# Kernel optimization log

Hardware: AMD Instinct MI355X
Metric: run time of the kernel (lower is better)

Reference implementation:

```python
import jax, jax.numpy as jnp
import numpy as np

NUM_GENES = 20000
NUM_CLASS = 32
BATCH_SIZE = 8
N = NUM_GENES * BATCH_SIZE      # 160_000 total nodes
E = 2_560_000                    # edges (avg degree 16)
K = 10
ALPHA = 0.1


def setup_inputs() -> dict:
    key = jax.random.key(0)
    ks = jax.random.split(key, 9)
    x = jax.random.normal(ks[0], (N, 1), dtype=jnp.float32)
    edge_index = jax.random.randint(ks[1], (2, E), 0, N, dtype=jnp.int32)
    batch = jnp.repeat(jnp.arange(BATCH_SIZE, dtype=jnp.int32), NUM_GENES)
    exp_emb_table = jax.random.normal(ks[2], (NUM_GENES, NUM_CLASS), dtype=jnp.float32) * 0.1
    exp_bias_table = jax.random.normal(ks[3], (NUM_GENES, 1), dtype=jnp.float32) * 0.1
    s = 1.0 / np.sqrt(NUM_CLASS)
    W1 = jax.random.uniform(ks[4], (NUM_CLASS, NUM_CLASS), jnp.float32, -s, s)
    b1 = jax.random.uniform(ks[5], (NUM_CLASS,), jnp.float32, -s, s)
    W2 = jax.random.uniform(ks[6], (NUM_CLASS, NUM_CLASS), jnp.float32, -s, s)
    b2 = jax.random.uniform(ks[7], (NUM_CLASS,), jnp.float32, -s, s)
    return {"x": x, "edge_index": edge_index, "batch": batch,
            "exp_emb_table": exp_emb_table, "exp_bias_table": exp_bias_table,
            "W1": W1, "b1": b1, "W2": W2, "b2": b2}


def reference(x, edge_index, batch, exp_emb_table, exp_bias_table, W1, b1, W2, b2):
    # node_index tiles 0..num_genes-1 for each graph in the batch
    node_index = jnp.tile(jnp.arange(NUM_GENES), BATCH_SIZE)        # [N]
    h = exp_emb_table[node_index] * x + exp_bias_table[node_index]  # [N, C]
    # dropout is identity in eval mode
    h = jax.nn.relu(h @ W1.T + b1)
    h = h @ W2.T + b2

    # APPNP: gcn_norm with self-loops, then k power-iteration steps
    loops = jnp.arange(N, dtype=edge_index.dtype)
    row = jnp.concatenate([edge_index[0], loops])  # source
    col = jnp.concatenate([edge_index[1], loops])  # target
    deg = jax.ops.segment_sum(jnp.ones_like(col, dtype=h.dtype), col, num_segments=N)
    dinv = jnp.where(deg > 0, jax.lax.rsqrt(deg), 0.0)
    norm = (dinv[row] * dinv[col])[:, None]        # [E+N, 1]

    h0 = h
    def step(carry, _):
        agg = jax.ops.segment_sum(carry[row] * norm, col, num_segments=N)
        return (1.0 - ALPHA) * agg + ALPHA * h0, None
    h, _ = jax.lax.scan(step, h, None, length=K)

    # global mean pool over graphs
    sums = jax.ops.segment_sum(h, batch, num_segments=BATCH_SIZE)
    counts = jax.ops.segment_sum(jnp.ones((N, 1), h.dtype), batch, num_segments=BATCH_SIZE)
    return sums / counts  # [BATCH_SIZE, NUM_CLASS]
```

## Files before the change

### kernel.cpp

```cpp
#include <hip/hip_runtime.h>

typedef unsigned int u32;
typedef unsigned short u16;

#define NPB 64
#define CNTB 512
#define MSEG 16
#define PCHUNK 4096
#define SPB 16
#define DHCHUNK 8
#define OUT_CHUNK 640

__device__ inline float bf2f(u16 b) { return __uint_as_float(((u32)b) << 16); }
__device__ inline u16 f2bf(float f) {
    u32 u = __float_as_uint(f);
    return (u16)((u + 0x7fffu + ((u >> 16) & 1u)) >> 16);
}
__device__ inline u32 pack2(float a, float b) { return (u32)f2bf(a) | ((u32)f2bf(b) << 16); }

__global__ void k_zero_i(int* __restrict__ p, int n) {
    int i = blockIdx.x * 256 + threadIdx.x;
    if (i < n) p[i] = 0;
}

__global__ void k_cnt(const int* __restrict__ ei, int E,
                      int* __restrict__ pcnt, int nbuckets) {
    extern __shared__ int h[];
    int M = nbuckets + 64;
    for (int i = threadIdx.x; i < M; i += 256) h[i] = 0;
    __syncthreads();
    int stride = gridDim.x * 256;
    for (int e = blockIdx.x * 256 + threadIdx.x; e < E; e += stride) {
        atomicAdd(&h[ei[e] >> 6], 1);
        atomicAdd(&h[nbuckets + (ei[E + e] >> 12)], 1);
    }
    __syncthreads();
    int* dst = pcnt + (size_t)blockIdx.x * M;
    for (int i = threadIdx.x; i < M; i += 256) dst[i] = h[i];
}

__global__ void k_merge(const int* __restrict__ pcnt, int M, int nbuckets,
                        int* __restrict__ bcnt, int* __restrict__ dscnt) {
    int bin = blockIdx.x * 256 + threadIdx.x;
    if (bin >= M) return;
    const int per = CNTB / MSEG;
    const int* p = pcnt + (size_t)(blockIdx.y * per) * M + bin;
    int s0 = 0, s1 = 0, s2 = 0, s3 = 0;
    #pragma unroll
    for (int b = 0; b < per; b += 4) {
        s0 += p[(size_t)(b + 0) * M];
        s1 += p[(size_t)(b + 1) * M];
        s2 += p[(size_t)(b + 2) * M];
        s3 += p[(size_t)(b + 3) * M];
    }
    int s = s0 + s1 + s2 + s3;
    if (s) {
        if (bin < nbuckets) atomicAdd(&bcnt[bin], s);
        else atomicAdd(&dscnt[bin - nbuckets], s);
    }
}

__global__ void k_scanB(const int* __restrict__ bcnt, int nbuckets,
                        const int* __restrict__ dscnt,
                        int* __restrict__ boff, int* __restrict__ bCur,
                        int* __restrict__ soff, int* __restrict__ sCur,
                        int* __restrict__ dsoff, int* __restrict__ dsCur,
                        int* __restrict__ offsets, int N, int E, int nsup, int nsupD) {
    __shared__ int s[1024];
    __shared__ int carry;
    int t = threadIdx.x;
    if (t == 0) carry = 0;
    __syncthreads();
    for (int base = 0; base < nbuckets; base += 1024) {
        int i = base + t;
        int v = (i < nbuckets) ? bcnt[i] : 0;
        s[t] = v;
        __syncthreads();
        for (int off = 1; off < 1024; off <<= 1) {
            int tmp = (t >= off) ? s[t - off] : 0;
            __syncthreads();
            s[t] += tmp;
            __syncthreads();
        }
        int pos = s[t] - v + carry;
        if (i < nbuckets) {
            boff[i] = pos;
            bCur[i] = pos;
            if ((i & 63) == 0) { soff[i >> 6] = pos; sCur[i >> 6] = pos; }
        }
        __syncthreads();
        if (t == 1023) carry += s[1023];
        __syncthreads();
    }
    if (t == 0) {
        boff[nbuckets] = E; soff[nsup] = E; offsets[N] = E;
        int acc = 0;
        for (int i = 0; i < nsupD; ++i) {
            dsoff[i] = acc; dsCur[i] = acc;
            acc += dscnt[i];
        }
        dsoff[nsupD] = E;
    }
}

__global__ __launch_bounds__(512) void k_part(const int* __restrict__ ei, int E,
                                              int* __restrict__ sCur, int* __restrict__ dsCur,
                                              u32* __restrict__ buf1, u16* __restrict__ dbuf) {
    __shared__ int cnt[64];
    __shared__ int cur[64];
    __shared__ int dcnt[64];
    __shared__ int dcur[64];
    int c0 = blockIdx.x * PCHUNK;
    int c1 = min(E, c0 + PCHUNK);
    int t = threadIdx.x;
    if (t < 64) { cnt[t] = 0; dcnt[t] = 0; }
    __syncthreads();
    for (int e = c0 + t; e < c1; e += 512) {
        atomicAdd(&cnt[ei[e] >> 12], 1);
        atomicAdd(&dcnt[ei[E + e] >> 12], 1);
    }
    __syncthreads();
    if (t < 64) {
        int c = cnt[t];
        cur[t] = c ? atomicAdd(&sCur[t], c) : 0;
        int dc = dcnt[t];
        dcur[t] = dc ? atomicAdd(&dsCur[t], dc) : 0;
    }
    __syncthreads();
    for (int e = c0 + t; e < c1; e += 512) {
        int s = ei[e];
        int d = ei[E + e];
        int p = atomicAdd(&cur[s >> 12], 1);
        buf1[p] = (u32)(d & 0x3FFFF) | ((u32)(s & 4095) << 18);
        int pd = atomicAdd(&dcur[d >> 12], 1);
        dbuf[pd] = (u16)(d & 4095);
    }
}

__global__ __launch_bounds__(256) void k_dhist(const u16* __restrict__ dbuf,
                                               const int* __restrict__ dsoff,
                                               int* __restrict__ deg, int N) {
    __shared__ int h[4096];
    int sup = blockIdx.x / DHCHUNK;
    int ch = blockIdx.x % DHCHUNK;
    int t = threadIdx.x;
    for (int i = t; i < 4096; i += 256) h[i] = 0;
    __syncthreads();
    int s0 = dsoff[sup], s1 = dsoff[sup + 1];
    int per = (s1 - s0 + DHCHUNK - 1) / DHCHUNK;
    int c0 = s0 + ch * per;
    int c1 = min(s1, c0 + per);
    for (int e = c0 + t; e < c1; e += 256)
        atomicAdd(&h[dbuf[e]], 1);
    __syncthreads();
    int vbase = sup << 12;
    for (int i = t; i < 4096; i += 256) {
        int v = h[i];
        if (v && vbase + i < N) atomicAdd(&deg[vbase + i], v);
    }
}

__global__ __launch_bounds__(256) void k_p2(const u32* __restrict__ buf1,
                                            const int* __restrict__ soff,
                                            int* __restrict__ bCur,
                                            u32* __restrict__ binned) {
    __shared__ int cnt[64];
    __shared__ int cur[64];
    int sb = blockIdx.x / SPB;
    int ch = blockIdx.x % SPB;
    int s0 = soff[sb], s1 = soff[sb + 1];
    int per = (s1 - s0 + SPB - 1) / SPB;
    int c0 = s0 + ch * per;
    int c1 = min(s1, c0 + per);
    int t = threadIdx.x;
    if (t < 64) cnt[t] = 0;
    __syncthreads();
    for (int e = c0 + t; e < c1; e += 256)
        atomicAdd(&cnt[(buf1[e] >> 24) & 63], 1);
    __syncthreads();
    if (t < 64) {
        int c = cnt[t];
        cur[t] = (c > 0) ? atomicAdd(&bCur[(sb << 6) + t], c) : 0;
    }
    __syncthreads();
    for (int e = c0 + t; e < c1; e += 256) {
        u32 v = buf1[e];
        int p = atomicAdd(&cur[(v >> 24) & 63], 1);
        binned[p] = v & 0x00FFFFFFu;
    }
}

__global__ __launch_bounds__(256) void k_sort(const u32* __restrict__ binned,
                                              const int* __restrict__ boff,
                                              int* __restrict__ offsets,
                                              int* __restrict__ dsts, int N) {
    __shared__ int cnt[64];
    __shared__ int off[64];
    int b = blockIdx.x;
    int s0 = boff[b], s1 = boff[b + 1];
    int t = threadIdx.x;
    if (t < 64) cnt[t] = 0;
    __syncthreads();
    for (int e = s0 + t; e < s1; e += 256)
        atomicAdd(&cnt[(binned[e] >> 18) & 63], 1);
    __syncthreads();
    if (t == 0) {
        int acc = s0;
        #pragma unroll
        for (int i = 0; i < 64; ++i) { off[i] = acc; acc += cnt[i]; }
    }
    __syncthreads();
    int vbase = b << 6;
    if (t < 64 && vbase + t < N) offsets[vbase + t] = off[t];
    __syncthreads();
    if (t < 64) cnt[t] = off[t];
    __syncthreads();
    for (int e = s0 + t; e < s1; e += 256) {
        u32 v = binned[e];
        int p = atomicAdd(&cnt[(v >> 18) & 63], 1);
        dsts[p] = (int)(v & 0x3FFFFu);
    }
}

__global__ __launch_bounds__(256) void k_AW(const float* __restrict__ emb,
                                            const float* __restrict__ W1,
                                            float* __restrict__ A,
                                            float* __restrict__ s1, int ngenes) {
    __shared__ float w1[32][33];
    __shared__ float eb[8][33];
    int t = threadIdx.x;
    int j = t & 31, gl = t >> 5;
    for (int i = t; i < 1024; i += 256) w1[i >> 5][i & 31] = W1[i];
    int g = blockIdx.x * 8 + gl;
    if (g < ngenes) eb[gl][j] = emb[g * 32 + j];
    __syncthreads();
    if (blockIdx.x == 0 && t < 32) {
        float acc = 0.f;
        #pragma unroll
        for (int c = 0; c < 32; ++c) acc += w1[t][c];
        s1[t] = acc;
    }
    if (g < ngenes) {
        float acc = 0.f;
        #pragma unroll
        for (int c = 0; c < 32; ++c) acc = fmaf(eb[gl][c], w1[j][c], acc);
        A[(size_t)g * 32 + j] = acc;
    }
}

__global__ __launch_bounds__(256) void k_h0(const float* __restrict__ x,
                                            const float* __restrict__ A,
                                            const float* __restrict__ bias,
                                            const float* __restrict__ s1,
                                            const float* __restrict__ b1,
                                            const float* __restrict__ W2,
                                            const float* __restrict__ b2,
                                            const int* __restrict__ deg,
                                            float* __restrict__ dinv,
                                            float* __restrict__ afac,
                                            float* __restrict__ rd,
                                            uint4* __restrict__ h0,
                                            uint4* __restrict__ q0,
                                            float* __restrict__ out, int out_n,
                                            int N, int ngenes) {
    int node = blockIdx.x * 256 + threadIdx.x;
    if (blockIdx.x == 0 && threadIdx.x < out_n) out[threadIdx.x] = 0.f;
    if (node >= N) return;
    float d = (float)(deg[node] + 1);
    float dv = rsqrtf(d);
    dinv[node] = dv;
    afac[node] = 0.9f * dv * dv;
    rd[node] = sqrtf(d);
    int g = node % ngenes;
    float xv = x[node];
    float bv = bias[g];
    const float4* Ar = (const float4*)(A + (size_t)g * 32);
    float r1[32];
    #pragma unroll
    for (int q = 0; q < 8; ++q) {
        float4 a4 = Ar[q];
        r1[q * 4 + 0] = fmaxf(fmaf(xv, a4.x, fmaf(bv, s1[q * 4 + 0], b1[q * 4 + 0])), 0.f);
        r1[q * 4 + 1] = fmaxf(fmaf(xv, a4.y, fmaf(bv, s1[q * 4 + 1], b1[q * 4 + 1])), 0.f);
        r1[q * 4 + 2] = fmaxf(fmaf(xv, a4.z, fmaf(bv, s1[q * 4 + 2], b1[q * 4 + 2])), 0.f);
        r1[q * 4 + 3] = fmaxf(fmaf(xv, a4.w, fmaf(bv, s1[q * 4 + 3], b1[q * 4 + 3])), 0.f);
    }
    u32 ow[16];
    #pragma unroll
    for (int i = 0; i < 32; i += 2) {
        float accA = b2[i];
        float accB = b2[i + 1];
        #pragma unroll
        for (int j2 = 0; j2 < 32; ++j2) {
            accA = fmaf(r1[j2], W2[i * 32 + j2], accA);
            accB = fmaf(r1[j2], W2[(i + 1) * 32 + j2], accB);
        }
        ow[i >> 1] = pack2(accA, accB);
    }
    #pragma unroll
    for (int q = 0; q < 4; ++q) {
        uint4 o;
        o.x = ow[q * 4 + 0];
        o.y = ow[q * 4 + 1];
        o.z = ow[q * 4 + 2];
        o.w = ow[q * 4 + 3];
        h0[(size_t)node * 4 + q] = o;
    }
    int gb = node / ngenes;
    u32 lo = (u32)f2bf(dv);
    u32 hi = lo << 16;
    uint4 qo;
    qo.x = (gb == 0) ? lo : (gb == 1) ? hi : 0u;
    qo.y = (gb == 2) ? lo : (gb == 3) ? hi : 0u;
    qo.z = (gb == 4) ? lo : (gb == 5) ? hi : 0u;
    qo.w = (gb == 6) ? lo : (gb == 7) ? hi : 0u;
    q0[node] = qo;
}

__device__ inline void qacc(const uint4& v, float& c0, float& c1, float& c2, float& c3,
                            float& c4, float& c5, float& c6, float& c7) {
    c0 += bf2f((u16)v.x); c1 += bf2f((u16)(v.x >> 16));
    c2 += bf2f((u16)v.y); c3 += bf2f((u16)(v.y >> 16));
    c4 += bf2f((u16)v.z); c5 += bf2f((u16)(v.z >> 16));
    c6 += bf2f((u16)v.w); c7 += bf2f((u16)(v.w >> 16));
}

__global__ __launch_bounds__(256) void k_prop8(const uint4* __restrict__ qin,
                                               uint4* __restrict__ qout,
                                               const float* __restrict__ a,
                                               const float* __restrict__ dinv,
                                               const int* __restrict__ offsets,
                                               const int* __restrict__ dsts,
                                               int N, int ngenes) {
    int node = blockIdx.x * 256 + threadIdx.x;
    if (node >= N) return;
    int s0 = offsets[node];
    int s1 = offsets[node + 1];
    uint4 self = qin[node];
    float c0 = bf2f((u16)self.x), c1 = bf2f((u16)(self.x >> 16));
    float c2 = bf2f((u16)self.y), c3 = bf2f((u16)(self.y >> 16));
    float c4 = bf2f((u16)self.z), c5 = bf2f((u16)(self.z >> 16));
    float c6 = bf2f((u16)self.w), c7 = bf2f((u16)(self.w >> 16));
    int e = s0;
    for (; e + 8 <= s1; e += 8) {
        int d0 = dsts[e + 0], d1 = dsts[e + 1], d2 = dsts[e + 2], d3 = dsts[e + 3];
        int d4 = dsts[e + 4], d5 = dsts[e + 5], d6 = dsts[e + 6], d7 = dsts[e + 7];
        uint4 v0 = qin[d0];
        uint4 v1 = qin[d1];
        uint4 v2 = qin[d2];
        uint4 v3 = qin[d3];
        uint4 v4 = qin[d4];
        uint4 v5 = qin[d5];
        uint4 v6 = qin[d6];
        uint4 v7 = qin[d7];
        qacc(v0, c0, c1, c2, c3, c4, c5, c6, c7);
        qacc(v1, c0, c1, c2, c3, c4, c5, c6, c7);
        qacc(v2, c0, c1, c2, c3, c4, c5, c6, c7);
        qacc(v3, c0, c1, c2, c3, c4, c5, c6, c7);
        qacc(v4, c0, c1, c2, c3, c4, c5, c6, c7);
        qacc(v5, c0, c1, c2, c3, c4, c5, c6, c7);
        qacc(v6, c0, c1, c2, c3, c4, c5, c6, c7);
        qacc(v7, c0, c1, c2, c3, c4, c5, c6, c7);
    }
    if (e + 4 <= s1) {
        int d0 = dsts[e + 0], d1 = dsts[e + 1], d2 = dsts[e + 2], d3 = dsts[e + 3];
        uint4 v0 = qin[d0];
        uint4 v1 = qin[d1];
        uint4 v2 = qin[d2];
        uint4 v3 = qin[d3];
        qacc(v0, c0, c1, c2, c3, c4, c5, c6, c7);
        qacc(v1, c0, c1, c2, c3, c4, c5, c6, c7);
        qacc(v2, c0, c1, c2, c3, c4, c5, c6, c7);
        qacc(v3, c0, c1, c2, c3, c4, c5, c6, c7);
        e += 4;
    }
    for (; e < s1; ++e) {
        uint4 v = qin[dsts[e]];
        qacc(v, c0, c1, c2, c3, c4, c5, c6, c7);
    }
    float av = a[node];
    float qi = 0.1f * dinv[node];
    int gb = node / ngenes;
    c0 = av * c0 + ((gb == 0) ? qi : 0.f);
    c1 = av * c1 + ((gb == 1) ? qi : 0.f);
    c2 = av * c2 + ((gb == 2) ? qi : 0.f);
    c3 = av * c3 + ((gb == 3) ? qi : 0.f);
    c4 = av * c4 + ((gb == 4) ? qi : 0.f);
    c5 = av * c5 + ((gb == 5) ? qi : 0.f);
    c6 = av * c6 + ((gb == 6) ? qi : 0.f);
    c7 = av * c7 + ((gb == 7) ? qi : 0.f);
    uint4 o;
    o.x = pack2(c0, c1);
    o.y = pack2(c2, c3);
    o.z = pack2(c4, c5);
    o.w = pack2(c6, c7);
    qout[node] = o;
}

__global__ __launch_bounds__(256) void k_out(const uint4* __restrict__ q,
                                             const u16* __restrict__ h0,
                                             const float* __restrict__ rd,
                                             float* __restrict__ out,
                                             int N, int ngenes) {
    __shared__ float wq[64][8];
    __shared__ u16 hs[64][32];
    int t = threadIdx.x;
    int b = t >> 5, c = t & 31;
    float acc = 0.f;
    int base = blockIdx.x * OUT_CHUNK;
    int lim = min(N, base + OUT_CHUNK);
    for (int v0 = base; v0 < lim; v0 += 64) {
        int nv = min(64, lim - v0);
        __syncthreads();
        int r = t >> 2, w4 = t & 3;
        if (r < nv) {
            *(uint4*)&hs[r][w4 * 8] = ((const uint4*)(h0 + (size_t)(v0 + r) * 32))[w4];
            u32 wv = ((const u32*)&q[v0 + r])[w4];
            float rdv = rd[v0 + r];
            wq[r][w4 * 2] = bf2f((u16)wv) * rdv;
            wq[r][w4 * 2 + 1] = bf2f((u16)(wv >> 16)) * rdv;
        }
        __syncthreads();
        for (int i = 0; i < nv; ++i)
            acc = fmaf(wq[i][b], bf2f(hs[i][c]), acc);
    }
    atomicAdd(&out[b * 32 + c], acc / (float)ngenes);
}

extern "C" void kernel_launch(void* const* d_in, const int* in_sizes, int n_in,
                              void* d_out, int out_size, void* d_ws, size_t ws_size,
                              hipStream_t stream) {
    const float* x    = (const float*)d_in[0];
    const int*   ei   = (const int*)d_in[1];
    const float* emb  = (const float*)d_in[3];
    const float* bias = (const float*)d_in[4];
    const float* W1   = (const float*)d_in[5];
    const float* b1   = (const float*)d_in[6];
    const float* W2   = (const float*)d_in[7];
    const float* b2   = (const float*)d_in[8];
    float* out = (float*)d_out;

    int N = in_sizes[0];
    int E = in_sizes[1] / 2;
    int ngenes = in_sizes[4];
    int nbuckets = (N + NPB - 1) / NPB;
    int nsup = (nbuckets + 63) / 64;
    int nsupD = (N + 4095) / 4096;
    int M = nbuckets + 64;

    char* pws = (char*)d_ws;
    auto carve = [&](size_t bytes) {
        void* r = (void*)pws;
        pws += (bytes + 255) & ~(size_t)255;
        return r;
    };
    u16*   h0      = (u16*)carve((size_t)N * 32 * 2);
    uint4* qA      = (uint4*)carve((size_t)N * 16);
    uint4* qB      = (uint4*)carve((size_t)N * 16);
    float* Amat    = (float*)carve((size_t)ngenes * 32 * 4);
    float* s1v     = (float*)carve(32 * 4);
    float* dinv    = (float*)carve((size_t)N * 4);
    float* afac    = (float*)carve((size_t)N * 4);
    float* rd      = (float*)carve((size_t)N * 4);
    int*   offsets = (int*)carve((size_t)(N + 1) * 4);
    int*   deg     = (int*)carve((size_t)N * 4);
    int*   bcnt    = (int*)carve((size_t)nbuckets * 4);
    int*   dscnt   = (int*)carve(64 * 4);
    int*   boff    = (int*)carve((size_t)(nbuckets + 1) * 4);
    int*   bCur    = (int*)carve((size_t)nbuckets * 4);
    int*   soff    = (int*)carve(65 * 4);
    int*   sCur    = (int*)carve(64 * 4);
    int*   dsoff   = (int*)carve(65 * 4);
    int*   dsCur   = (int*)carve(64 * 4);
    int*   pcnt    = (int*)carve((size_t)CNTB * M * 4);
    u32*   buf1    = (u32*)carve((size_t)E * 4);
    u32*   binned  = (u32*)carve((size_t)E * 4);
    int*   dsts    = (int*)carve((size_t)E * 4);
    u16*   dbuf    = (u16*)carve((size_t)E * 2);

    int nbN = (N + 255) / 256;
    int zlen = (int)(dscnt - deg) + 64;

    hipLaunchKernelGGL(k_zero_i, dim3((zlen + 255) / 256), dim3(256), 0, stream, deg, zlen);
    hipLaunchKernelGGL(k_cnt, dim3(CNTB), dim3(256), M * 4, stream, ei, E, pcnt, nbuckets);
    hipLaunchKernelGGL(k_merge, dim3((M + 255) / 256, MSEG), dim3(256), 0, stream,
                       pcnt, M, nbuckets, bcnt, dscnt);
    hipLaunchKernelGGL(k_scanB, dim3(1), dim3(1024), 0, stream,
                       bcnt, nbuckets, dscnt, boff, bCur, soff, sCur, dsoff, dsCur,
                       offsets, N, E, nsup, nsupD);
    hipLaunchKernelGGL(k_part, dim3((E + PCHUNK - 1) / PCHUNK), dim3(512), 0, stream,
                       ei, E, sCur, dsCur, buf1, dbuf);
    hipLaunchKernelGGL(k_dhist, dim3(nsupD * DHCHUNK), dim3(256), 0, stream,
                       dbuf, dsoff, deg, N);
    hipLaunchKernelGGL(k_p2, dim3(nsup * SPB), dim3(256), 0, stream, buf1, soff, bCur, binned);
    hipLaunchKernelGGL(k_sort, dim3(nbuckets), dim3(256), 0, stream,
                       binned, boff, offsets, dsts, N);
    hipLaunchKernelGGL(k_AW, dim3((ngenes + 7) / 8), dim3(256), 0, stream, emb, W1, Amat, s1v, ngenes);
    hipLaunchKernelGGL(k_h0, dim3(nbN), dim3(256), 0, stream,
                       x, Amat, bias, s1v, b1, W2, b2, deg, dinv, afac, rd,
                       (uint4*)h0, qA, out, out_size, N, ngenes);

    const uint4* qin = qA;
    for (int it = 0; it < 10; ++it) {
        uint4* qo = (it & 1) ? qA : qB;
        hipLaunchKernelGGL(k_prop8, dim3(nbN), dim3(256), 0, stream,
                           qin, qo, afac, dinv, offsets, dsts, N, ngenes);
        qin = qo;
    }

    hipLaunchKernelGGL(k_out, dim3((N + OUT_CHUNK - 1) / OUT_CHUNK), dim3(256), 0, stream,
                       qin, h0, rd, out, N, ngenes);
}
```

Before: 351.9 us.

## Remove zero and AW kernels, vectorize edge loads, merge per-node coefficients

Removes the zeroing kernel and the separate emb·W1 precompute kernel, folding the W1 product into k_h0 per node. Merge and degree histogram now write results directly instead of using atomics, so no zero-init is needed. Edge loads in the count, partition and prop kernels switch to int4 vector loads. dinv and afac are packed into a single float2 array to cut per-node loads in propagation. This lowers launch count and memory traffic but adds redundant 32x32 FMA work per node in k_h0 and reduces parallelism in merge and dhist.

```diff
diff --git a/kernel.cpp b/kernel.cpp
--- a/kernel.cpp
+++ b/kernel.cpp
@@ -5,10 +5,8 @@
 
 #define NPB 64
 #define CNTB 512
-#define MSEG 16
 #define PCHUNK 4096
 #define SPB 16
-#define DHCHUNK 8
 #define OUT_CHUNK 640
 
 __device__ inline float bf2f(u16 b) { return __uint_as_float(((u32)b) << 16); }
@@ -18,21 +16,32 @@
 }
 __device__ inline u32 pack2(float a, float b) { return (u32)f2bf(a) | ((u32)f2bf(b) << 16); }
 
-__global__ void k_zero_i(int* __restrict__ p, int n) {
-    int i = blockIdx.x * 256 + threadIdx.x;
-    if (i < n) p[i] = 0;
-}
-
-__global__ void k_cnt(const int* __restrict__ ei, int E,
-                      int* __restrict__ pcnt, int nbuckets) {
+__global__ void k_cnt(const int4* __restrict__ s4, const int4* __restrict__ d4,
+                      int n4, int E, int* __restrict__ pcnt, int nbuckets) {
     extern __shared__ int h[];
     int M = nbuckets + 64;
     for (int i = threadIdx.x; i < M; i += 256) h[i] = 0;
     __syncthreads();
     int stride = gridDim.x * 256;
-    for (int e = blockIdx.x * 256 + threadIdx.x; e < E; e += stride) {
-        atomicAdd(&h[ei[e] >> 6], 1);
-        atomicAdd(&h[nbuckets + (ei[E + e] >> 12)], 1);
+    for (int i = blockIdx.x * 256 + threadIdx.x; i < n4; i += stride) {
+        int4 s = s4[i];
+        int4 d = d4[i];
+        atomicAdd(&h[s.x >> 6], 1);
+        atomicAdd(&h[s.y >> 6], 1);
+        atomicAdd(&h[s.z >> 6], 1);
+        atomicAdd(&h[s.w >> 6], 1);
+        atomicAdd(&h[nbuckets + (d.x >> 12)], 1);
+        atomicAdd(&h[nbuckets + (d.y >> 12)], 1);
+        atomicAdd(&h[nbuckets + (d.z >> 12)], 1);
+        atomicAdd(&h[nbuckets + (d.w >> 12)], 1);
+    }
+    if (blockIdx.x == 0 && threadIdx.x == 0) {
+        const int* si = (const int*)s4;
+        const int* di = (const int*)d4;
+        for (int e = n4 * 4; e < E; ++e) {
+            atomicAdd(&h[si[e] >> 6], 1);
+            atomicAdd(&h[nbuckets + (di[e] >> 12)], 1);
+        }
     }
     __syncthreads();
     int* dst = pcnt + (size_t)blockIdx.x * M;
@@ -43,21 +52,19 @@
                         int* __restrict__ bcnt, int* __restrict__ dscnt) {
     int bin = blockIdx.x * 256 + threadIdx.x;
     if (bin >= M) return;
-    const int per = CNTB / MSEG;
-    const int* p = pcnt + (size_t)(blockIdx.y * per) * M + bin;
-    int s0 = 0, s1 = 0, s2 = 0, s3 = 0;
-    #pragma unroll
-    for (int b = 0; b < per; b += 4) {
-        s0 += p[(size_t)(b + 0) * M];
-        s1 += p[(size_t)(b + 1) * M];
-        s2 += p[(size_t)(b + 2) * M];
-        s3 += p[(size_t)(b + 3) * M];
-    }
-    int s = s0 + s1 + s2 + s3;
-    if (s) {
-        if (bin < nbuckets) atomicAdd(&bcnt[bin], s);
-        else atomicAdd(&dscnt[bin - nbuckets], s);
-    }
+    const int* p = pcnt + bin;
+    int a[16];
+    #pragma unroll
+    for (int k = 0; k < 16; ++k) a[k] = 0;
+    for (int b = 0; b < CNTB; b += 16) {
+        #pragma unroll
+        for (int k = 0; k < 16; ++k) a[k] += p[(size_t)(b + k) * M];
+    }
+    int s = 0;
+    #pragma unroll
+    for (int k = 0; k < 16; ++k) s += a[k];
+    if (bin < nbuckets) bcnt[bin] = s;
+    else dscnt[bin - nbuckets] = s;
 }
 
 __global__ void k_scanB(const int* __restrict__ bcnt, int nbuckets,
@@ -103,6 +110,23 @@
     }
 }
 
+__device__ inline void ldgrp(const int* __restrict__ ei, int E, int e0,
+                             int* s, int* d) {
+    if (e0 + 3 < E) {
+        int4 sv = *(const int4*)(ei + e0);
+        int4 dv = *(const int4*)(ei + E + e0);
+        s[0] = sv.x; s[1] = sv.y; s[2] = sv.z; s[3] = sv.w;
+        d[0] = dv.x; d[1] = dv.y; d[2] = dv.z; d[3] = dv.w;
+    } else {
+        #pragma unroll
+        for (int k = 0; k < 4; ++k) {
+            int e = e0 + k;
+            if (e < E) { s[k] = ei[e]; d[k] = ei[E + e]; }
+            else       { s[k] = -1;    d[k] = 0; }
+        }
+    }
+}
+
 __global__ __launch_bounds__(512) void k_part(const int* __restrict__ ei, int E,
                                               int* __restrict__ sCur, int* __restrict__ dsCur,
                                               u32* __restrict__ buf1, u16* __restrict__ dbuf) {
@@ -110,14 +134,17 @@
     __shared__ int cur[64];
     __shared__ int dcnt[64];
     __shared__ int dcur[64];
-    int c0 = blockIdx.x * PCHUNK;
-    int c1 = min(E, c0 + PCHUNK);
     int t = threadIdx.x;
     if (t < 64) { cnt[t] = 0; dcnt[t] = 0; }
     __syncthreads();
-    for (int e = c0 + t; e < c1; e += 512) {
-        atomicAdd(&cnt[ei[e] >> 12], 1);
-        atomicAdd(&dcnt[ei[E + e] >> 12], 1);
+    int c0 = blockIdx.x * PCHUNK;
+    int sA[4], dA[4], sB[4], dB[4];
+    ldgrp(ei, E, c0 + 4 * t, sA, dA);
+    ldgrp(ei, E, c0 + 2048 + 4 * t, sB, dB);
+    #pragma unroll
+    for (int k = 0; k < 4; ++k) {
+        if (sA[k] >= 0) { atomicAdd(&cnt[sA[k] >> 12], 1); atomicAdd(&dcnt[dA[k] >> 12], 1); }
+        if (sB[k] >= 0) { atomicAdd(&cnt[sB[k] >> 12], 1); atomicAdd(&dcnt[dB[k] >> 12], 1); }
     }
     __syncthreads();
     if (t < 64) {
@@ -127,37 +154,38 @@
         dcur[t] = dc ? atomicAdd(&dsCur[t], dc) : 0;
     }
     __syncthreads();
-    for (int e = c0 + t; e < c1; e += 512) {
-        int s = ei[e];
-        int d = ei[E + e];
-        int p = atomicAdd(&cur[s >> 12], 1);
-        buf1[p] = (u32)(d & 0x3FFFF) | ((u32)(s & 4095) << 18);
-        int pd = atomicAdd(&dcur[d >> 12], 1);
-        dbuf[pd] = (u16)(d & 4095);
-    }
-}
-
-__global__ __launch_bounds__(256) void k_dhist(const u16* __restrict__ dbuf,
+    #pragma unroll
+    for (int k = 0; k < 4; ++k) {
+        if (sA[k] >= 0) {
+            int p = atomicAdd(&cur[sA[k] >> 12], 1);
+            buf1[p] = (u32)(dA[k] & 0x3FFFF) | ((u32)(sA[k] & 4095) << 18);
+            int pd = atomicAdd(&dcur[dA[k] >> 12], 1);
+            dbuf[pd] = (u16)(dA[k] & 4095);
+        }
+        if (sB[k] >= 0) {
+            int p = atomicAdd(&cur[sB[k] >> 12], 1);
+            buf1[p] = (u32)(dB[k] & 0x3FFFF) | ((u32)(sB[k] & 4095) << 18);
+            int pd = atomicAdd(&dcur[dB[k] >> 12], 1);
+            dbuf[pd] = (u16)(dB[k] & 4095);
+        }
+    }
+}
+
+__global__ __launch_bounds__(512) void k_dhist(const u16* __restrict__ dbuf,
                                                const int* __restrict__ dsoff,
                                                int* __restrict__ deg, int N) {
     __shared__ int h[4096];
-    int sup = blockIdx.x / DHCHUNK;
-    int ch = blockIdx.x % DHCHUNK;
+    int sup = blockIdx.x;
     int t = threadIdx.x;
-    for (int i = t; i < 4096; i += 256) h[i] = 0;
+    for (int i = t; i < 4096; i += 512) h[i] = 0;
     __syncthreads();
     int s0 = dsoff[sup], s1 = dsoff[sup + 1];
-    int per = (s1 - s0 + DHCHUNK - 1) / DHCHUNK;
-    int c0 = s0 + ch * per;
-    int c1 = min(s1, c0 + per);
-    for (int e = c0 + t; e < c1; e += 256)
+    for (int e = s0 + t; e < s1; e += 512)
         atomicAdd(&h[dbuf[e]], 1);
     __syncthreads();
     int vbase = sup << 12;
-    for (int i = t; i < 4096; i += 256) {
-        int v = h[i];
-        if (v && vbase + i < N) atomicAdd(&deg[vbase + i], v);
-    }
+    for (int i = t; i < 4096; i += 512)
+        if (vbase + i < N) deg[vbase + i] = h[i];
 }
 
 __global__ __launch_bounds__(256) void k_p2(const u32* __restrict__ buf1,
@@ -222,42 +250,15 @@
     }
 }
 
-__global__ __launch_bounds__(256) void k_AW(const float* __restrict__ emb,
+__global__ __launch_bounds__(256) void k_h0(const float* __restrict__ x,
+                                            const float* __restrict__ emb,
+                                            const float* __restrict__ bias,
                                             const float* __restrict__ W1,
-                                            float* __restrict__ A,
-                                            float* __restrict__ s1, int ngenes) {
-    __shared__ float w1[32][33];
-    __shared__ float eb[8][33];
-    int t = threadIdx.x;
-    int j = t & 31, gl = t >> 5;
-    for (int i = t; i < 1024; i += 256) w1[i >> 5][i & 31] = W1[i];
-    int g = blockIdx.x * 8 + gl;
-    if (g < ngenes) eb[gl][j] = emb[g * 32 + j];
-    __syncthreads();
-    if (blockIdx.x == 0 && t < 32) {
-        float acc = 0.f;
-        #pragma unroll
-        for (int c = 0; c < 32; ++c) acc += w1[t][c];
-        s1[t] = acc;
-    }
-    if (g < ngenes) {
-        float acc = 0.f;
-        #pragma unroll
-        for (int c = 0; c < 32; ++c) acc = fmaf(eb[gl][c], w1[j][c], acc);
-        A[(size_t)g * 32 + j] = acc;
-    }
-}
-
-__global__ __launch_bounds__(256) void k_h0(const float* __restrict__ x,
-                                            const float* __restrict__ A,
-                                            const float* __restrict__ bias,
-                                            const float* __restrict__ s1,
                                             const float* __restrict__ b1,
                                             const float* __restrict__ W2,
                                             const float* __restrict__ b2,
                                             const int* __restrict__ deg,
-                                            float* __restrict__ dinv,
-                                            float* __restrict__ afac,
+                                            float2* __restrict__ coef,
                                             float* __restrict__ rd,
                                             uint4* __restrict__ h0,
                                             uint4* __restrict__ q0,
@@ -268,21 +269,32 @@
     if (node >= N) return;
     float d = (float)(deg[node] + 1);
     float dv = rsqrtf(d);
-    dinv[node] = dv;
-    afac[node] = 0.9f * dv * dv;
+    coef[node] = make_float2(0.9f * dv * dv, 0.1f * dv);
     rd[node] = sqrtf(d);
     int g = node % ngenes;
     float xv = x[node];
     float bv = bias[g];
-    const float4* Ar = (const float4*)(A + (size_t)g * 32);
+    float er[32];
+    {
+        const float4* e4 = (const float4*)(emb + (size_t)g * 32);
+        #pragma unroll
+        for (int q = 0; q < 8; ++q) {
+            float4 v = e4[q];
+            er[q * 4 + 0] = v.x; er[q * 4 + 1] = v.y;
+            er[q * 4 + 2] = v.z; er[q * 4 + 3] = v.w;
+        }
+    }
     float r1[32];
     #pragma unroll
-    for (int q = 0; q < 8; ++q) {
-        float4 a4 = Ar[q];
-        r1[q * 4 + 0] = fmaxf(fmaf(xv, a4.x, fmaf(bv, s1[q * 4 + 0], b1[q * 4 + 0])), 0.f);
-        r1[q * 4 + 1] = fmaxf(fmaf(xv, a4.y, fmaf(bv, s1[q * 4 + 1], b1[q * 4 + 1])), 0.f);
-        r1[q * 4 + 2] = fmaxf(fmaf(xv, a4.z, fmaf(bv, s1[q * 4 + 2], b1[q * 4 + 2])), 0.f);
-        r1[q * 4 + 3] = fmaxf(fmaf(xv, a4.w, fmaf(bv, s1[q * 4 + 3], b1[q * 4 + 3])), 0.f);
+    for (int j = 0; j < 32; ++j) {
+        float a = 0.f, s = 0.f;
+        #pragma unroll
+        for (int c = 0; c < 32; ++c) {
+            float w = W1[j * 32 + c];
+            a = fmaf(er[c], w, a);
+            s += w;
+        }
+        r1[j] = fmaxf(fmaf(xv, a, fmaf(bv, s, b1[j])), 0.f);
     }
     u32 ow[16];
     #pragma unroll
@@ -326,8 +338,7 @@
 
 __global__ __launch_bounds__(256) void k_prop8(const uint4* __restrict__ qin,
                                                uint4* __restrict__ qout,
-                                               const float* __restrict__ a,
-                                               const float* __restrict__ dinv,
+                                               const float2* __restrict__ coef,
                                                const int* __restrict__ offsets,
                                                const int* __restrict__ dsts,
                                                int N, int ngenes) {
@@ -341,17 +352,19 @@
     float c4 = bf2f((u16)self.z), c5 = bf2f((u16)(self.z >> 16));
     float c6 = bf2f((u16)self.w), c7 = bf2f((u16)(self.w >> 16));
     int e = s0;
+    for (; e < s1 && (e & 3); ++e)
+        qacc(qin[dsts[e]], c0, c1, c2, c3, c4, c5, c6, c7);
     for (; e + 8 <= s1; e += 8) {
-        int d0 = dsts[e + 0], d1 = dsts[e + 1], d2 = dsts[e + 2], d3 = dsts[e + 3];
-        int d4 = dsts[e + 4], d5 = dsts[e + 5], d6 = dsts[e + 6], d7 = dsts[e + 7];
-        uint4 v0 = qin[d0];
-        uint4 v1 = qin[d1];
-        uint4 v2 = qin[d2];
-        uint4 v3 = qin[d3];
-        uint4 v4 = qin[d4];
-        uint4 v5 = qin[d5];
-        uint4 v6 = qin[d6];
-        uint4 v7 = qin[d7];
+        int4 da = *(const int4*)&dsts[e];
+        int4 db = *(const int4*)&dsts[e + 4];
+        uint4 v0 = qin[da.x];
+        uint4 v1 = qin[da.y];
+        uint4 v2 = qin[da.z];
+        uint4 v3 = qin[da.w];
+        uint4 v4 = qin[db.x];
+        uint4 v5 = qin[db.y];
+        uint4 v6 = qin[db.z];
+        uint4 v7 = qin[db.w];
         qacc(v0, c0, c1, c2, c3, c4, c5, c6, c7);
         qacc(v1, c0, c1, c2, c3, c4, c5, c6, c7);
         qacc(v2, c0, c1, c2, c3, c4, c5, c6, c7);
@@ -362,23 +375,21 @@
         qacc(v7, c0, c1, c2, c3, c4, c5, c6, c7);
     }
     if (e + 4 <= s1) {
-        int d0 = dsts[e + 0], d1 = dsts[e + 1], d2 = dsts[e + 2], d3 = dsts[e + 3];
-        uint4 v0 = qin[d0];
-        uint4 v1 = qin[d1];
-        uint4 v2 = qin[d2];
-        uint4 v3 = qin[d3];
+        int4 da = *(const int4*)&dsts[e];
+        uint4 v0 = qin[da.x];
+        uint4 v1 = qin[da.y];
+        uint4 v2 = qin[da.z];
+        uint4 v3 = qin[da.w];
         qacc(v0, c0, c1, c2, c3, c4, c5, c6, c7);
         qacc(v1, c0, c1, c2, c3, c4, c5, c6, c7);
         qacc(v2, c0, c1, c2, c3, c4, c5, c6, c7);
         qacc(v3, c0, c1, c2, c3, c4, c5, c6, c7);
         e += 4;
     }
-    for (; e < s1; ++e) {
-        uint4 v = qin[dsts[e]];
-        qacc(v, c0, c1, c2, c3, c4, c5, c6, c7);
-    }
-    float av = a[node];
-    float qi = 0.1f * dinv[node];
+    for (; e < s1; ++e)
+        qacc(qin[dsts[e]], c0, c1, c2, c3, c4, c5, c6, c7);
+    float2 cf = coef[node];
+    float av = cf.x, qi = cf.y;
     int gb = node / ngenes;
     c0 = av * c0 + ((gb == 0) ? qi : 0.f);
     c1 = av * c1 + ((gb == 1) ? qi : 0.f);
@@ -453,57 +464,51 @@
         pws += (bytes + 255) & ~(size_t)255;
         return r;
     };
-    u16*   h0      = (u16*)carve((size_t)N * 32 * 2);
-    uint4* qA      = (uint4*)carve((size_t)N * 16);
-    uint4* qB      = (uint4*)carve((size_t)N * 16);
-    float* Amat    = (float*)carve((size_t)ngenes * 32 * 4);
-    float* s1v     = (float*)carve(32 * 4);
-    float* dinv    = (float*)carve((size_t)N * 4);
-    float* afac    = (float*)carve((size_t)N * 4);
-    float* rd      = (float*)carve((size_t)N * 4);
-    int*   offsets = (int*)carve((size_t)(N + 1) * 4);
-    int*   deg     = (int*)carve((size_t)N * 4);
-    int*   bcnt    = (int*)carve((size_t)nbuckets * 4);
-    int*   dscnt   = (int*)carve(64 * 4);
-    int*   boff    = (int*)carve((size_t)(nbuckets + 1) * 4);
-    int*   bCur    = (int*)carve((size_t)nbuckets * 4);
-    int*   soff    = (int*)carve(65 * 4);
-    int*   sCur    = (int*)carve(64 * 4);
-    int*   dsoff   = (int*)carve(65 * 4);
-    int*   dsCur   = (int*)carve(64 * 4);
-    int*   pcnt    = (int*)carve((size_t)CNTB * M * 4);
-    u32*   buf1    = (u32*)carve((size_t)E * 4);
-    u32*   binned  = (u32*)carve((size_t)E * 4);
-    int*   dsts    = (int*)carve((size_t)E * 4);
-    u16*   dbuf    = (u16*)carve((size_t)E * 2);
+    u16*    h0      = (u16*)carve((size_t)N * 32 * 2);
+    uint4*  qA      = (uint4*)carve((size_t)N * 16);
+    uint4*  qB      = (uint4*)carve((size_t)N * 16);
+    float2* coef    = (float2*)carve((size_t)N * 8);
+    float*  rd      = (float*)carve((size_t)N * 4);
+    int*    offsets = (int*)carve((size_t)(N + 1) * 4);
+    int*    deg     = (int*)carve((size_t)N * 4);
+    int*    bcnt    = (int*)carve((size_t)nbuckets * 4);
+    int*    dscnt   = (int*)carve(64 * 4);
+    int*    boff    = (int*)carve((size_t)(nbuckets + 1) * 4);
+    int*    bCur    = (int*)carve((size_t)nbuckets * 4);
+    int*    soff    = (int*)carve(65 * 4);
+    int*    sCur    = (int*)carve(64 * 4);
+    int*    dsoff   = (int*)carve(65 * 4);
+    int*    dsCur   = (int*)carve(64 * 4);
+    int*    pcnt    = (int*)carve((size_t)CNTB * M * 4);
+    u32*    buf1    = (u32*)carve((size_t)E * 4);
+    u32*    binned  = (u32*)carve((size_t)E * 4);
+    int*    dsts    = (int*)carve((size_t)E * 4);
+    u16*    dbuf    = (u16*)carve((size_t)E * 2);
 
     int nbN = (N + 255) / 256;
-    int zlen = (int)(dscnt - deg) + 64;
-
-    hipLaunchKernelGGL(k_zero_i, dim3((zlen + 255) / 256), dim3(256), 0, stream, deg, zlen);
-    hipLaunchKernelGGL(k_cnt, dim3(CNTB), dim3(256), M * 4, stream, ei, E, pcnt, nbuckets);
-    hipLaunchKernelGGL(k_merge, dim3((M + 255) / 256, MSEG), dim3(256), 0, stream,
+
+    hipLaunchKernelGGL(k_cnt, dim3(CNTB), dim3(256), M * 4, stream,
+                       (const int4*)ei, (const int4*)(ei + E), E / 4, E, pcnt, nbuckets);
+    hipLaunchKernelGGL(k_merge, dim3((M + 255) / 256), dim3(256), 0, stream,
                        pcnt, M, nbuckets, bcnt, dscnt);
     hipLaunchKernelGGL(k_scanB, dim3(1), dim3(1024), 0, stream,
                        bcnt, nbuckets, dscnt, boff, bCur, soff, sCur, dsoff, dsCur,
                        offsets, N, E, nsup, nsupD);
     hipLaunchKernelGGL(k_part, dim3((E + PCHUNK - 1) / PCHUNK), dim3(512), 0, stream,
                        ei, E, sCur, dsCur, buf1, dbuf);
-    hipLaunchKernelGGL(k_dhist, dim3(nsupD * DHCHUNK), dim3(256), 0, stream,
-                       dbuf, dsoff, deg, N);
+    hipLaunchKernelGGL(k_dhist, dim3(nsupD), dim3(512), 0, stream, dbuf, dsoff, deg, N);
     hipLaunchKernelGGL(k_p2, dim3(nsup * SPB), dim3(256), 0, stream, buf1, soff, bCur, binned);
     hipLaunchKernelGGL(k_sort, dim3(nbuckets), dim3(256), 0, stream,
                        binned, boff, offsets, dsts, N);
-    hipLaunchKernelGGL(k_AW, dim3((ngenes + 7) / 8), dim3(256), 0, stream, emb, W1, Amat, s1v, ngenes);
     hipLaunchKernelGGL(k_h0, dim3(nbN), dim3(256), 0, stream,
-                       x, Amat, bias, s1v, b1, W2, b2, deg, dinv, afac, rd,
+                       x, emb, bias, W1, b1, W2, b2, deg, coef, rd,
                        (uint4*)h0, qA, out, out_size, N, ngenes);
 
     const uint4* qin = qA;
     for (int it = 0; it < 10; ++it) {
         uint4* qo = (it & 1) ? qA : qB;
         hipLaunchKernelGGL(k_prop8, dim3(nbN), dim3(256), 0, stream,
-                           qin, qo, afac, dinv, offsets, dsts, N, ngenes);
+                           qin, qo, coef, offsets, dsts, N, ngenes);
         qin = qo;
     }
 
```

New measurement: 382.4 us. 1.09x slower.
